# Optimization experiments

Hardware: AMD Instinct MI355X
Metric: run time of the kernel (lower is better)

The kernel has to match this reference:

```python
import jax, jax.numpy as jnp
import numpy as np

C = 1.0                      # ball curvature c
SQRT_C = 1.0                 # sqrt(c)
EPS = 1e-15                  # norm clamp
BALL_EPS = 1e-5              # projection margin
B, DIN, DOUT = 262144, 128, 128


def artanh(u):
    u = jnp.clip(u, -1.0 + 1e-7, 1.0 - 1e-7)
    return 0.5 * (jnp.log1p(u) - jnp.log1p(-u))


def mobius_matvec(W, x):
    # x: [B, din], W: [dout, din]
    x_norm = jnp.clip(jnp.linalg.norm(x, axis=-1, keepdims=True), EPS)
    Mx = x @ W.T                                   # [B, dout]
    Mx_norm = jnp.clip(jnp.linalg.norm(Mx, axis=-1, keepdims=True), EPS)
    scale = jnp.tanh(Mx_norm / x_norm * artanh(SQRT_C * x_norm)) / (Mx_norm * SQRT_C)
    res = scale * Mx
    return jnp.where(Mx_norm <= 1e-10, 0.0, res)


def mobius_add(x, y):
    # x: [B, d], y broadcastable to [B, d]
    x2 = jnp.sum(x * x, axis=-1, keepdims=True)
    y2 = jnp.sum(y * y, axis=-1, keepdims=True)
    xy = jnp.sum(x * y, axis=-1, keepdims=True)
    num = (1.0 + 2.0 * C * xy + C * y2) * x + (1.0 - C * x2) * y
    den = jnp.clip(1.0 + 2.0 * C * xy + C * C * x2 * y2, EPS)
    return num / den


def projx(x):
    norm = jnp.clip(jnp.linalg.norm(x, axis=-1, keepdims=True), EPS)
    maxnorm = (1.0 - BALL_EPS) / SQRT_C
    return jnp.where(norm > maxnorm, x / norm * maxnorm, x)


def setup_inputs() -> dict:
    key = jax.random.key(0)
    k1, k2, k3 = jax.random.split(key, 3)
    # points strictly inside the unit ball: randn * 0.05 -> norm ~ 0.57 max tail-safe
    x = jax.random.normal(k1, (B, DIN), dtype=jnp.float32) * 0.05
    fan = np.sqrt(6.0 / (DIN + DOUT))  # xavier_uniform scale
    weight = jax.random.uniform(k2, (DOUT, DIN), dtype=jnp.float32, minval=-fan, maxval=fan)
    bias = jax.random.normal(k3, (DOUT,), dtype=jnp.float32) * 0.05
    return {"x": x, "weight": weight, "bias": bias}


def reference(x, weight, bias):
    y = mobius_matvec(weight, x)
    y = mobius_add(y, bias[None, :])
    return projx(y)
```

## Files before the change

kernel.cpp:

```cpp
#include <hip/hip_runtime.h>

typedef __attribute__((ext_vector_type(8))) short short8;
typedef __attribute__((ext_vector_type(4))) float floatx4;

__device__ __forceinline__ unsigned short f2b(float f) {
    union { float f; unsigned int i; } v; v.f = f;
    unsigned int u = v.i;
    u += 0x7FFFu + ((u >> 16) & 1u);
    return (unsigned short)(u >> 16);
}

#define NTILES 2048
#define GRID   1024

__global__ __launch_bounds__(256, 3) void mobius_linear_kernel(
    const float* __restrict__ X,
    const float* __restrict__ W,
    const float* __restrict__ Bias,
    float* __restrict__ Out)
{
    __shared__ unsigned short ldsW[128 * 136];
    __shared__ float ldsB[128];

    const int tid  = threadIdx.x;
    const int wave = tid >> 6;
    const int lane = tid & 63;
    const int q = lane >> 4;
    const int c = lane & 15;

#pragma unroll
    for (int i = 0; i < 8; ++i) {
        int chunk = i * 256 + tid;
        int row = chunk >> 4, cc = chunk & 15;
        const float* src = W + row * 128 + cc * 8;
        floatx4 w0 = *reinterpret_cast<const floatx4*>(src);
        floatx4 w1 = *reinterpret_cast<const floatx4*>(src + 4);
        short8 pk;
#pragma unroll
        for (int j = 0; j < 4; ++j) { pk[j] = (short)f2b(w0[j]); pk[4 + j] = (short)f2b(w1[j]); }
        *reinterpret_cast<short8*>(&ldsW[row * 136 + cc * 8]) = pk;
    }
    if (tid < 32)
        *reinterpret_cast<floatx4*>(&ldsB[tid * 4]) =
            *reinterpret_cast<const floatx4*>(Bias + tid * 4);

    __syncthreads();

    float b2 = 0.f;
#pragma unroll
    for (int n = 0; n < 8; ++n) {
        floatx4 bv = *reinterpret_cast<const floatx4*>(&ldsB[n * 16 + q * 4]);
#pragma unroll
        for (int r = 0; r < 4; ++r) b2 = fmaf(bv[r], bv[r], b2);
    }
    b2 += __shfl_xor(b2, 16); b2 += __shfl_xor(b2, 32);

    for (int t = blockIdx.x; t < NTILES; t += gridDim.x) {
        const int rowbase = t * 128 + wave * 32;

        short8 xfrag[2][4];
        float xn2[2] = {0.f, 0.f};
#pragma unroll
        for (int g = 0; g < 2; ++g) {
            const float* xrow = X + (size_t)(rowbase + g * 16 + c) * 128;
#pragma unroll
            for (int kc = 0; kc < 4; ++kc) {
                const floatx4* src = reinterpret_cast<const floatx4*>(xrow + kc * 32 + q * 8);
                floatx4 x0 = __builtin_nontemporal_load(src);
                floatx4 x1 = __builtin_nontemporal_load(src + 1);
                short8 pk;
#pragma unroll
                for (int j = 0; j < 4; ++j) {
                    xn2[g] = fmaf(x0[j], x0[j], xn2[g]);
                    xn2[g] = fmaf(x1[j], x1[j], xn2[g]);
                    pk[j] = (short)f2b(x0[j]); pk[4 + j] = (short)f2b(x1[j]);
                }
                xfrag[g][kc] = pk;
            }
        }
        xn2[0] += __shfl_xor(xn2[0], 16); xn2[0] += __shfl_xor(xn2[0], 32);
        xn2[1] += __shfl_xor(xn2[1], 16); xn2[1] += __shfl_xor(xn2[1], 32);

        floatx4 acc[2][8];
#pragma unroll
        for (int g = 0; g < 2; ++g)
#pragma unroll
            for (int n = 0; n < 8; ++n)
                acc[g][n] = (floatx4){0.f, 0.f, 0.f, 0.f};

#pragma unroll
        for (int kc = 0; kc < 4; ++kc) {
#pragma unroll
            for (int n = 0; n < 8; ++n) {
                short8 wf = *reinterpret_cast<const short8*>(
                    &ldsW[(n * 16 + c) * 136 + kc * 32 + q * 8]);
                acc[0][n] = __builtin_amdgcn_mfma_f32_16x16x32_bf16(wf, xfrag[0][kc], acc[0][n], 0, 0, 0);
                acc[1][n] = __builtin_amdgcn_mfma_f32_16x16x32_bf16(wf, xfrag[1][kc], acc[1][n], 0, 0, 0);
            }
        }

        floatx4 bfr[8];
#pragma unroll
        for (int n = 0; n < 8; ++n)
            bfr[n] = *reinterpret_cast<const floatx4*>(&ldsB[n * 16 + q * 4]);

#pragma unroll
        for (int g = 0; g < 2; ++g) {
            float m2 = 0.f, mbv = 0.f;
#pragma unroll
            for (int n = 0; n < 8; ++n)
#pragma unroll
                for (int r = 0; r < 4; ++r) {
                    float v = acc[g][n][r];
                    m2  = fmaf(v, v, m2);
                    mbv = fmaf(v, bfr[n][r], mbv);
                }
            m2  += __shfl_xor(m2, 16);  m2  += __shfl_xor(m2, 32);
            mbv += __shfl_xor(mbv, 16); mbv += __shfl_xor(mbv, 32);

            float xnorm = fmaxf(sqrtf(xn2[g]), 1e-15f);
            float u     = fminf(xnorm, 1.f - 1e-7f);
            float at    = 0.5f * __logf((1.f + u) / (1.f - u));
            float Mxn   = fmaxf(sqrtf(m2), 1e-15f);
            float arg   = Mxn / xnorm * at;
            float e     = __expf(2.f * arg);
            float th    = 1.f - 2.f / (e + 1.f);
            float scale = (Mxn <= 1e-10f) ? 0.f : th / Mxn;
            float y2 = scale * scale * m2;
            float yb = scale * mbv;
            float t1  = 1.f + 2.f * yb + b2;
            float den = fmaxf(fmaf(y2, b2, 1.f + 2.f * yb), 1e-15f);
            float Af = t1 * scale / den;
            float Bf = (1.f - y2) / den;
            float zn2 = Af * Af * m2 + 2.f * Af * Bf * mbv + Bf * Bf * b2;
            float zn  = fmaxf(sqrtf(zn2), 1e-15f);
            const float maxn = 1.f - 1e-5f;
            float fac = (zn > maxn) ? (maxn / zn) : 1.f;
            Af *= fac; Bf *= fac;

            float* orow = Out + (size_t)(rowbase + g * 16 + c) * 128;
#pragma unroll
            for (int n = 0; n < 8; ++n) {
                floatx4 o;
#pragma unroll
                for (int r = 0; r < 4; ++r)
                    o[r] = fmaf(Af, acc[g][n][r], Bf * bfr[n][r]);
                __builtin_nontemporal_store(o, reinterpret_cast<floatx4*>(orow + n * 16 + q * 4));
            }
        }
    }
}

extern "C" void kernel_launch(void* const* d_in, const int* in_sizes, int n_in,
                              void* d_out, int out_size, void* d_ws, size_t ws_size,
                              hipStream_t stream) {
    const float* X    = (const float*)d_in[0];
    const float* W    = (const float*)d_in[1];
    const float* Bias = (const float*)d_in[2];
    float* Out = (float*)d_out;

    dim3 grid(GRID), block(256);
    hipLaunchKernelGGL(mobius_linear_kernel, grid, block, 0, stream, X, W, Bias, Out);
}
```

Before: 308.2 us.

## Prefetch next X tile during epilogue and raise occupancy bound

Software-pipelines the persistent tile loop: the first X tile is loaded before the weight staging, and the next tile's X fragments are loaded and converted right after the MFMAs so their latency overlaps the epilogue math and stores. Bias fragments are reloaded from LDS inside the epilogue instead of held in registers, and launch bounds rise from 3 to 4 blocks per CU. Output stores switch from nontemporal to regular. The prefetch adds register pressure, which works against the higher occupancy target and may cause spills.

```diff
diff --git a/kernel.cpp b/kernel.cpp
--- a/kernel.cpp
+++ b/kernel.cpp
@@ -13,7 +13,7 @@
 #define NTILES 2048
 #define GRID   1024
 
-__global__ __launch_bounds__(256, 3) void mobius_linear_kernel(
+__global__ __launch_bounds__(256, 4) void mobius_linear_kernel(
     const float* __restrict__ X,
     const float* __restrict__ W,
     const float* __restrict__ Bias,
@@ -27,6 +27,40 @@
     const int lane = tid & 63;
     const int q = lane >> 4;
     const int c = lane & 15;
+
+    int t = blockIdx.x;
+    short8 xfrag[2][4];
+    float xn2[2];
+
+#define LOADX(T)                                                              \
+    {                                                                         \
+        const int rb_ = (T) * 128 + wave * 32;                                \
+        xn2[0] = 0.f; xn2[1] = 0.f;                                           \
+        _Pragma("unroll")                                                     \
+        for (int g = 0; g < 2; ++g) {                                         \
+            const float* xrow = X + (size_t)(rb_ + g * 16 + c) * 128;         \
+            _Pragma("unroll")                                                 \
+            for (int kc = 0; kc < 4; ++kc) {                                  \
+                const floatx4* src =                                          \
+                    reinterpret_cast<const floatx4*>(xrow + kc * 32 + q * 8); \
+                floatx4 x0 = __builtin_nontemporal_load(src);                 \
+                floatx4 x1 = __builtin_nontemporal_load(src + 1);             \
+                short8 pk;                                                    \
+                _Pragma("unroll")                                             \
+                for (int j = 0; j < 4; ++j) {                                 \
+                    xn2[g] = fmaf(x0[j], x0[j], xn2[g]);                      \
+                    xn2[g] = fmaf(x1[j], x1[j], xn2[g]);                      \
+                    pk[j] = (short)f2b(x0[j]);                                \
+                    pk[4 + j] = (short)f2b(x1[j]);                            \
+                }                                                             \
+                xfrag[g][kc] = pk;                                            \
+            }                                                                 \
+        }                                                                     \
+        xn2[0] += __shfl_xor(xn2[0], 16); xn2[0] += __shfl_xor(xn2[0], 32);   \
+        xn2[1] += __shfl_xor(xn2[1], 16); xn2[1] += __shfl_xor(xn2[1], 32);   \
+    }
+
+    LOADX(t);
 
 #pragma unroll
     for (int i = 0; i < 8; ++i) {
@@ -55,32 +89,7 @@
     }
     b2 += __shfl_xor(b2, 16); b2 += __shfl_xor(b2, 32);
 
-    for (int t = blockIdx.x; t < NTILES; t += gridDim.x) {
-        const int rowbase = t * 128 + wave * 32;
-
-        short8 xfrag[2][4];
-        float xn2[2] = {0.f, 0.f};
-#pragma unroll
-        for (int g = 0; g < 2; ++g) {
-            const float* xrow = X + (size_t)(rowbase + g * 16 + c) * 128;
-#pragma unroll
-            for (int kc = 0; kc < 4; ++kc) {
-                const floatx4* src = reinterpret_cast<const floatx4*>(xrow + kc * 32 + q * 8);
-                floatx4 x0 = __builtin_nontemporal_load(src);
-                floatx4 x1 = __builtin_nontemporal_load(src + 1);
-                short8 pk;
-#pragma unroll
-                for (int j = 0; j < 4; ++j) {
-                    xn2[g] = fmaf(x0[j], x0[j], xn2[g]);
-                    xn2[g] = fmaf(x1[j], x1[j], xn2[g]);
-                    pk[j] = (short)f2b(x0[j]); pk[4 + j] = (short)f2b(x1[j]);
-                }
-                xfrag[g][kc] = pk;
-            }
-        }
-        xn2[0] += __shfl_xor(xn2[0], 16); xn2[0] += __shfl_xor(xn2[0], 32);
-        xn2[1] += __shfl_xor(xn2[1], 16); xn2[1] += __shfl_xor(xn2[1], 32);
-
+    for (;;) {
         floatx4 acc[2][8];
 #pragma unroll
         for (int g = 0; g < 2; ++g)
@@ -99,26 +108,31 @@
             }
         }
 
-        floatx4 bfr[8];
-#pragma unroll
-        for (int n = 0; n < 8; ++n)
-            bfr[n] = *reinterpret_cast<const floatx4*>(&ldsB[n * 16 + q * 4]);
+        const int rowbase = t * 128 + wave * 32;
+        const float cx0 = xn2[0], cx1 = xn2[1];
+
+        const int tn = t + GRID;
+        const bool more = (tn < NTILES);
+        if (more) LOADX(tn);
 
 #pragma unroll
         for (int g = 0; g < 2; ++g) {
             float m2 = 0.f, mbv = 0.f;
 #pragma unroll
-            for (int n = 0; n < 8; ++n)
+            for (int n = 0; n < 8; ++n) {
+                floatx4 bv = *reinterpret_cast<const floatx4*>(&ldsB[n * 16 + q * 4]);
 #pragma unroll
                 for (int r = 0; r < 4; ++r) {
                     float v = acc[g][n][r];
                     m2  = fmaf(v, v, m2);
-                    mbv = fmaf(v, bfr[n][r], mbv);
+                    mbv = fmaf(v, bv[r], mbv);
                 }
+            }
             m2  += __shfl_xor(m2, 16);  m2  += __shfl_xor(m2, 32);
             mbv += __shfl_xor(mbv, 16); mbv += __shfl_xor(mbv, 32);
 
-            float xnorm = fmaxf(sqrtf(xn2[g]), 1e-15f);
+            float xr2   = (g == 0) ? cx0 : cx1;
+            float xnorm = fmaxf(sqrtf(xr2), 1e-15f);
             float u     = fminf(xnorm, 1.f - 1e-7f);
             float at    = 0.5f * __logf((1.f + u) / (1.f - u));
             float Mxn   = fmaxf(sqrtf(m2), 1e-15f);
@@ -141,14 +155,19 @@
             float* orow = Out + (size_t)(rowbase + g * 16 + c) * 128;
 #pragma unroll
             for (int n = 0; n < 8; ++n) {
+                floatx4 bv = *reinterpret_cast<const floatx4*>(&ldsB[n * 16 + q * 4]);
                 floatx4 o;
 #pragma unroll
                 for (int r = 0; r < 4; ++r)
-                    o[r] = fmaf(Af, acc[g][n][r], Bf * bfr[n][r]);
-                __builtin_nontemporal_store(o, reinterpret_cast<floatx4*>(orow + n * 16 + q * 4));
+                    o[r] = fmaf(Af, acc[g][n][r], Bf * bv[r]);
+                *reinterpret_cast<floatx4*>(orow + n * 16 + q * 4) = o;
             }
         }
+
+        if (!more) break;
+        t = tn;
     }
+#undef LOADX
 }
 
 extern "C" void kernel_launch(void* const* d_in, const int* in_sizes, int n_in,
```

Result: slower. 347.8 us (+12.9%).

## Prefetch second tile's X before first epilogue and overlap W staging

Applied to the files above, without the earlier changes.

Unrolls the persistent loop into exactly two tiles per block and issues the second tile's X loads before running the first tile's epilogue, so the global loads overlap with compute and stores. Odd blocks load their first X tile before staging W, even blocks after, to stagger memory traffic. Output stores change from nontemporal to regular. The kernel now assumes NTILES equals 2*GRID and holds two X fragment sets live, which raises register pressure and may reduce occupancy.

```diff
diff --git a/kernel.cpp b/kernel.cpp
--- a/kernel.cpp
+++ b/kernel.cpp
@@ -28,18 +28,54 @@
     const int q = lane >> 4;
     const int c = lane & 15;
 
+    auto loadx = [&](int T, short8 (&xf)[2][4], float (&xn)[2]) {
+        const int rb = T * 128 + wave * 32;
+        xn[0] = 0.f; xn[1] = 0.f;
 #pragma unroll
-    for (int i = 0; i < 8; ++i) {
-        int chunk = i * 256 + tid;
-        int row = chunk >> 4, cc = chunk & 15;
-        const float* src = W + row * 128 + cc * 8;
-        floatx4 w0 = *reinterpret_cast<const floatx4*>(src);
-        floatx4 w1 = *reinterpret_cast<const floatx4*>(src + 4);
-        short8 pk;
+        for (int g = 0; g < 2; ++g) {
+            const float* xrow = X + (size_t)(rb + g * 16 + c) * 128;
 #pragma unroll
-        for (int j = 0; j < 4; ++j) { pk[j] = (short)f2b(w0[j]); pk[4 + j] = (short)f2b(w1[j]); }
-        *reinterpret_cast<short8*>(&ldsW[row * 136 + cc * 8]) = pk;
-    }
+            for (int kc = 0; kc < 4; ++kc) {
+                const floatx4* src = reinterpret_cast<const floatx4*>(xrow + kc * 32 + q * 8);
+                floatx4 x0 = __builtin_nontemporal_load(src);
+                floatx4 x1 = __builtin_nontemporal_load(src + 1);
+                short8 pk;
+#pragma unroll
+                for (int j = 0; j < 4; ++j) {
+                    xn[g] = fmaf(x0[j], x0[j], xn[g]);
+                    xn[g] = fmaf(x1[j], x1[j], xn[g]);
+                    pk[j] = (short)f2b(x0[j]); pk[4 + j] = (short)f2b(x1[j]);
+                }
+                xf[g][kc] = pk;
+            }
+        }
+        xn[0] += __shfl_xor(xn[0], 16); xn[0] += __shfl_xor(xn[0], 32);
+        xn[1] += __shfl_xor(xn[1], 16); xn[1] += __shfl_xor(xn[1], 32);
+    };
+
+    auto stage_w = [&]() {
+#pragma unroll
+        for (int i = 0; i < 8; ++i) {
+            int chunk = i * 256 + tid;
+            int row = chunk >> 4, cc = chunk & 15;
+            const float* src = W + row * 128 + cc * 8;
+            floatx4 w0 = *reinterpret_cast<const floatx4*>(src);
+            floatx4 w1 = *reinterpret_cast<const floatx4*>(src + 4);
+            short8 pk;
+#pragma unroll
+            for (int j = 0; j < 4; ++j) { pk[j] = (short)f2b(w0[j]); pk[4 + j] = (short)f2b(w1[j]); }
+            *reinterpret_cast<short8*>(&ldsW[row * 136 + cc * 8]) = pk;
+        }
+    };
+
+    short8 xfA[2][4], xfB[2][4];
+    float xnA[2], xnB[2];
+    const int t0 = blockIdx.x;
+    const int t1 = blockIdx.x + GRID;
+
+    if (blockIdx.x & 1) { loadx(t0, xfA, xnA); stage_w(); }
+    else                { stage_w(); loadx(t0, xfA, xnA); }
+
     if (tid < 32)
         *reinterpret_cast<floatx4*>(&ldsB[tid * 4]) =
             *reinterpret_cast<const floatx4*>(Bias + tid * 4);
@@ -55,55 +91,32 @@
     }
     b2 += __shfl_xor(b2, 16); b2 += __shfl_xor(b2, 32);
 
-    for (int t = blockIdx.x; t < NTILES; t += gridDim.x) {
-        const int rowbase = t * 128 + wave * 32;
+    floatx4 acc[2][8];
 
-        short8 xfrag[2][4];
-        float xn2[2] = {0.f, 0.f};
-#pragma unroll
-        for (int g = 0; g < 2; ++g) {
-            const float* xrow = X + (size_t)(rowbase + g * 16 + c) * 128;
-#pragma unroll
-            for (int kc = 0; kc < 4; ++kc) {
-                const floatx4* src = reinterpret_cast<const floatx4*>(xrow + kc * 32 + q * 8);
-                floatx4 x0 = __builtin_nontemporal_load(src);
-                floatx4 x1 = __builtin_nontemporal_load(src + 1);
-                short8 pk;
-#pragma unroll
-                for (int j = 0; j < 4; ++j) {
-                    xn2[g] = fmaf(x0[j], x0[j], xn2[g]);
-                    xn2[g] = fmaf(x1[j], x1[j], xn2[g]);
-                    pk[j] = (short)f2b(x0[j]); pk[4 + j] = (short)f2b(x1[j]);
-                }
-                xfrag[g][kc] = pk;
-            }
-        }
-        xn2[0] += __shfl_xor(xn2[0], 16); xn2[0] += __shfl_xor(xn2[0], 32);
-        xn2[1] += __shfl_xor(xn2[1], 16); xn2[1] += __shfl_xor(xn2[1], 32);
-
-        floatx4 acc[2][8];
+    auto mfma_all = [&](short8 (&xf)[2][4]) {
 #pragma unroll
         for (int g = 0; g < 2; ++g)
 #pragma unroll
             for (int n = 0; n < 8; ++n)
                 acc[g][n] = (floatx4){0.f, 0.f, 0.f, 0.f};
-
 #pragma unroll
         for (int kc = 0; kc < 4; ++kc) {
 #pragma unroll
             for (int n = 0; n < 8; ++n) {
                 short8 wf = *reinterpret_cast<const short8*>(
                     &ldsW[(n * 16 + c) * 136 + kc * 32 + q * 8]);
-                acc[0][n] = __builtin_amdgcn_mfma_f32_16x16x32_bf16(wf, xfrag[0][kc], acc[0][n], 0, 0, 0);
-                acc[1][n] = __builtin_amdgcn_mfma_f32_16x16x32_bf16(wf, xfrag[1][kc], acc[1][n], 0, 0, 0);
+                acc[0][n] = __builtin_amdgcn_mfma_f32_16x16x32_bf16(wf, xf[0][kc], acc[0][n], 0, 0, 0);
+                acc[1][n] = __builtin_amdgcn_mfma_f32_16x16x32_bf16(wf, xf[1][kc], acc[1][n], 0, 0, 0);
             }
         }
+    };
 
+    auto epilogue = [&](int T, float (&xn)[2]) {
+        const int rb = T * 128 + wave * 32;
         floatx4 bfr[8];
 #pragma unroll
         for (int n = 0; n < 8; ++n)
             bfr[n] = *reinterpret_cast<const floatx4*>(&ldsB[n * 16 + q * 4]);
-
 #pragma unroll
         for (int g = 0; g < 2; ++g) {
             float m2 = 0.f, mbv = 0.f;
@@ -118,7 +131,7 @@
             m2  += __shfl_xor(m2, 16);  m2  += __shfl_xor(m2, 32);
             mbv += __shfl_xor(mbv, 16); mbv += __shfl_xor(mbv, 32);
 
-            float xnorm = fmaxf(sqrtf(xn2[g]), 1e-15f);
+            float xnorm = fmaxf(sqrtf(xn[g]), 1e-15f);
             float u     = fminf(xnorm, 1.f - 1e-7f);
             float at    = 0.5f * __logf((1.f + u) / (1.f - u));
             float Mxn   = fmaxf(sqrtf(m2), 1e-15f);
@@ -128,9 +141,9 @@
             float scale = (Mxn <= 1e-10f) ? 0.f : th / Mxn;
             float y2 = scale * scale * m2;
             float yb = scale * mbv;
-            float t1  = 1.f + 2.f * yb + b2;
+            float t1v = 1.f + 2.f * yb + b2;
             float den = fmaxf(fmaf(y2, b2, 1.f + 2.f * yb), 1e-15f);
-            float Af = t1 * scale / den;
+            float Af = t1v * scale / den;
             float Bf = (1.f - y2) / den;
             float zn2 = Af * Af * m2 + 2.f * Af * Bf * mbv + Bf * Bf * b2;
             float zn  = fmaxf(sqrtf(zn2), 1e-15f);
@@ -138,17 +151,23 @@
             float fac = (zn > maxn) ? (maxn / zn) : 1.f;
             Af *= fac; Bf *= fac;
 
-            float* orow = Out + (size_t)(rowbase + g * 16 + c) * 128;
+            float* orow = Out + (size_t)(rb + g * 16 + c) * 128;
 #pragma unroll
             for (int n = 0; n < 8; ++n) {
                 floatx4 o;
 #pragma unroll
                 for (int r = 0; r < 4; ++r)
                     o[r] = fmaf(Af, acc[g][n][r], Bf * bfr[n][r]);
-                __builtin_nontemporal_store(o, reinterpret_cast<floatx4*>(orow + n * 16 + q * 4));
+                *reinterpret_cast<floatx4*>(orow + n * 16 + q * 4) = o;
             }
         }
-    }
+    };
+
+    mfma_all(xfA);
+    loadx(t1, xfB, xnB);
+    epilogue(t0, xnA);
+    mfma_all(xfB);
+    epilogue(t1, xnB);
 }
 
 extern "C" void kernel_launch(void* const* d_in, const int* in_sizes, int n_in,
```

New measurement: 259.3 us. -15.9%, faster.
